# Kernel tuning notes

Measured on AMD Instinct MI355X. Metric: run time of the kernel, lower is better.

Reference implementation:

```python
import jax, jax.numpy as jnp
import numpy as np

NUM_LATENT, NUM_TRASH, DEPTH = 7, 3, 4
N_QUBITS = NUM_LATENT + NUM_TRASH            # 10, embedding/entangler wires
N_WIRES = NUM_LATENT + 2 * NUM_TRASH + 1     # 14, total device wires (wire 0 = MSB, PennyLane convention)
AUX = N_WIRES - 1                            # swap-test ancilla (last wire)
BATCH = 256

_H = (np.array([[1.0, 1.0], [1.0, -1.0]]) / np.sqrt(2.0)).astype(np.complex64)
_CNOT = np.array([[1, 0, 0, 0], [0, 1, 0, 0], [0, 0, 0, 1], [0, 0, 1, 0]], dtype=np.complex64)
_CSWAP = np.eye(8, dtype=np.complex64)
_CSWAP[[5, 6]] = _CSWAP[[6, 5]]              # swap targets iff control=1: |101> <-> |110>


def _rx(theta):
    # RX(theta) = [[cos(t/2), -i sin(t/2)], [-i sin(t/2), cos(t/2)]]; theta [...] -> [..., 2, 2]
    c = jnp.cos(theta / 2).astype(jnp.complex64)
    s = jnp.sin(theta / 2).astype(jnp.complex64) * (-1j)
    return jnp.stack([jnp.stack([c, s], -1), jnp.stack([s, c], -1)], -2)


def _apply_1q(state, gate, wire):
    # state [B, 2^W]; gate [2,2] (shared) or [B,2,2] (per-sample)
    B = state.shape[0]
    a, b = 2 ** wire, 2 ** (N_WIRES - wire - 1)
    s = state.reshape(B, a, 2, b)
    if gate.ndim == 3:
        s = jnp.einsum('bij,bajc->baic', gate, s)
    else:
        s = jnp.einsum('ij,bajc->baic', gate, s)
    return s.reshape(B, -1)


def _apply_kq(state, gate, wires):
    # general k-qubit constant gate on arbitrary (possibly non-adjacent) wires
    B = state.shape[0]
    k = len(wires)
    t = state.reshape((B,) + (2,) * N_WIRES)
    t = jnp.moveaxis(t, [w + 1 for w in wires], range(1, k + 1))
    t = t.reshape(B, 2 ** k, -1)
    t = jnp.einsum('ij,bjc->bic', jnp.asarray(gate), t)
    t = t.reshape((B,) + (2,) * N_WIRES)
    t = jnp.moveaxis(t, range(1, k + 1), [w + 1 for w in wires])
    return t.reshape(B, -1)


def _forward(features, weights):
    B = features.shape[0]
    state = jnp.zeros((B, 2 ** N_WIRES), jnp.complex64).at[:, 0].set(1.0)
    # AngleEmbedding(rotation='X'): per-sample RX(features[:, w]) on wire w
    g_emb = _rx(features)  # [B, n_qubits, 2, 2]
    for w in range(N_QUBITS):
        state = _apply_1q(state, g_emb[:, w], w)
    # BasicEntanglerLayers: per layer, RX(weights[l, w]) on each wire, then ring of CNOTs
    wts = weights.reshape(DEPTH, N_QUBITS)
    for l in range(DEPTH):
        g_l = _rx(wts[l])  # [n_qubits, 2, 2]
        for w in range(N_QUBITS):
            state = _apply_1q(state, g_l[w], w)
        for w in range(N_QUBITS):
            state = _apply_kq(state, _CNOT, [w, (w + 1) % N_QUBITS])
    # Swap test: H(aux); CSWAP(aux, latent+i, latent+trash+i); H(aux)
    state = _apply_1q(state, jnp.asarray(_H), AUX)
    for i in range(NUM_TRASH):
        state = _apply_kq(state, _CSWAP, [AUX, NUM_LATENT + i, NUM_LATENT + NUM_TRASH + i])
    state = _apply_1q(state, jnp.asarray(_H), AUX)
    # probs on aux wire (last wire -> innermost axis); return P(aux=1)
    p = jnp.sum(jnp.abs(state.reshape(B, 2 ** (N_WIRES - 1), 2)) ** 2, axis=1)
    return p[:, 1]


def setup_inputs() -> dict:
    key = jax.random.key(0)
    kf, kw = jax.random.split(key)
    features = jax.random.normal(kf, (BATCH, N_QUBITS), jnp.float32)
    weights = 0.01 * jax.random.uniform(kw, (DEPTH, N_QUBITS), jnp.float32)
    return {"features": features, "weights": weights}


def reference(features, weights):
    return _forward(features, weights)
```

## Files before the change

### kernel.cpp

```cpp
#include <hip/hip_runtime.h>
#include <math.h>


#define NQ     10
#define DEPTHL 4
#define NGATE  (NQ + DEPTHL * NQ)

constexpr int lfwd_step(int i) {
    for (int w = 0; w < NQ; ++w) {
        int cb = (i >> (NQ - 1 - w)) & 1;
        i ^= cb << (NQ - 1 - ((w + 1) % NQ));
    }
    return i;
}
constexpr int linv_step(int i) {
    for (int w = NQ - 1; w >= 0; --w) {
        int cb = (i >> (NQ - 1 - w)) & 1;
        i ^= cb << (NQ - 1 - ((w + 1) % NQ));
    }
    return i;
}

static_assert(lfwd_step(linv_step(0x155)) == 0x155, "linv must invert lfwd");
static_assert(linv_step(lfwd_step(0x2AB)) == 0x2AB, "lfwd must invert linv");

struct MaskTab { int m[NGATE]; int row[3]; };

constexpr MaskTab make_masks() {
    MaskTab M{};
    for (int w = 0; w < NQ; ++w) M.m[w] = 1 << (NQ - 1 - w);
    for (int l = 0; l < DEPTHL; ++l)
        for (int w = 0; w < NQ; ++w) {
            int v = 1 << (NQ - 1 - w);
            for (int k = 0; k < l; ++k) v = linv_step(v);
            M.m[NQ + NQ * l + w] = v;
        }
    for (int p = 0; p < 3; ++p) {
        int r = 0;
        for (int j = 0; j < NQ; ++j) {
            int y = 1 << j;
            for (int k = 0; k < DEPTHL; ++k) y = lfwd_step(y);
            r |= ((y >> p) & 1) << j;
        }
        M.row[p] = r;
    }
    return M;
}

constexpr MaskTab MK = make_masks();

constexpr bool masks_ok() {
    for (int g = 0; g < NGATE; ++g)
        if (MK.m[g] <= 0 || MK.m[g] > 1023) return false;
    return MK.row[0] && MK.row[1] && MK.row[2];
}
static_assert(masks_ok(), "gate masks must be nonzero 10-bit");

__global__ __launch_bounds__(64) void qae_kernel(
    const float* __restrict__ features,
    const float* __restrict__ weights,
    float* __restrict__ out)
{
    const int b    = blockIdx.x;
    const int lane = threadIdx.x;

    float cg = 1.0f, sg = 0.0f;
    if (lane < NGATE) {
        float ang = (lane < NQ) ? features[b * NQ + lane] : weights[lane - NQ];
        float h = 0.5f * ang;
        cg = cosf(h);
        sg = sinf(h);
    }

    float tre[16], tim[16];
#pragma unroll
    for (int r = 0; r < 16; ++r) { tre[r] = 0.0f; tim[r] = 0.0f; }
    if (lane == 0) tre[0] = 1.0f;

#pragma unroll
    for (int g = 0; g < NGATE; ++g) {
        const int v  = MK.m[g];
        const int lm = v >> 4;
        const int rm = v & 15;
        const float c = __shfl(cg, g, 64);
        const float s = __shfl(sg, g, 64);

        float pre[16], pim[16];
        if (lm) {
#pragma unroll
            for (int r = 0; r < 16; ++r) {
                pre[r] = __shfl_xor(tre[r ^ rm], lm, 64);
                pim[r] = __shfl_xor(tim[r ^ rm], lm, 64);
            }
        } else {
#pragma unroll
            for (int r = 0; r < 16; ++r) {
                pre[r] = tre[r ^ rm];
                pim[r] = tim[r ^ rm];
            }
        }
#pragma unroll
        for (int r = 0; r < 16; ++r) {
            tre[r] = fmaf(c, tre[r],  s * pim[r]);
            tim[r] = fmaf(c, tim[r], -s * pre[r]);
        }
    }

    const int pl0 = __popc((MK.row[0] >> 4) & lane) & 1;
    const int pl1 = __popc((MK.row[1] >> 4) & lane) & 1;
    const int pl2 = __popc((MK.row[2] >> 4) & lane) & 1;

    float acc = 0.0f;
#pragma unroll
    for (int r = 0; r < 16; ++r) {
        const int pr0 = __popc(MK.row[0] & 15 & r) & 1;
        const int pr1 = __popc(MK.row[1] & 15 & r) & 1;
        const int pr2 = __popc(MK.row[2] & 15 & r) & 1;
        const int bad = (pl0 ^ pr0) | (pl1 ^ pr1) | (pl2 ^ pr2);
        if (!bad) acc += tre[r] * tre[r] + tim[r] * tim[r];
    }

#pragma unroll
    for (int off = 32; off; off >>= 1)
        acc += __shfl_xor(acc, off, 64);

    if (lane == 0) out[b] = 0.5f * (1.0f - acc);
}

extern "C" void kernel_launch(void* const* d_in, const int* in_sizes, int n_in,
                              void* d_out, int out_size, void* d_ws, size_t ws_size,
                              hipStream_t stream) {
    const float* features = (const float*)d_in[0];
    const float* weights  = (const float*)d_in[1];
    float*       out      = (float*)d_out;

    int B = in_sizes[0] / NQ;
    qae_kernel<<<B, 64, 0, stream>>>(features, weights, out);
}
```

Measured before the change: 64.67 us.

## Replace sequential gate simulation with closed-form phase computation in Fourier basis

Instead of applying fifty RX gates one after another with cross-lane shuffles, the kernel computes each basis amplitude's phase directly as a signed sum of the rotation angles, using parity masks, followed by one sincos per amplitude. It then folds the three measurement parity rows with a few xor-shuffle butterfly additions before summing the squared magnitudes with a normalization factor. This removes about fifty rounds of 32 shuffles plus FMAs, at the cost of per-lane popcount/sign arithmetic and 16 sincos calls. It depends on the Fourier-domain identity holding exactly, and any numerical drift in the phase sums could affect accuracy.

```diff
diff --git a/kernel.cpp b/kernel.cpp
--- a/kernel.cpp
+++ b/kernel.cpp
@@ -4,7 +4,7 @@
 
 #define NQ     10
 #define DEPTHL 4
-#define NGATE  (NQ + DEPTHL * NQ)
+#define NSLOT  (NQ + DEPTHL * NQ)
 
 constexpr int lfwd_step(int i) {
     for (int w = 0; w < NQ; ++w) {
@@ -20,11 +20,10 @@
     }
     return i;
 }
-
 static_assert(lfwd_step(linv_step(0x155)) == 0x155, "linv must invert lfwd");
 static_assert(linv_step(lfwd_step(0x2AB)) == 0x2AB, "lfwd must invert linv");
 
-struct MaskTab { int m[NGATE]; int row[3]; };
+struct MaskTab { int m[NSLOT]; int row[3]; };
 
 constexpr MaskTab make_masks() {
     MaskTab M{};
@@ -46,15 +45,20 @@
     }
     return M;
 }
-
 constexpr MaskTab MK = make_masks();
 
 constexpr bool masks_ok() {
-    for (int g = 0; g < NGATE; ++g)
+    for (int g = 0; g < NSLOT; ++g)
         if (MK.m[g] <= 0 || MK.m[g] > 1023) return false;
     return MK.row[0] && MK.row[1] && MK.row[2];
 }
 static_assert(masks_ok(), "gate masks must be nonzero 10-bit");
+
+constexpr bool rows_indep() {
+    int a = MK.row[0], b = MK.row[1], c = MK.row[2];
+    return a && b && c && (a ^ b) && (a ^ c) && (b ^ c) && (a ^ b ^ c);
+}
+static_assert(rows_indep(), "measurement rows must be linearly independent");
 
 __global__ __launch_bounds__(64) void qae_kernel(
     const float* __restrict__ features,
@@ -64,67 +68,66 @@
     const int b    = blockIdx.x;
     const int lane = threadIdx.x;
 
-    float cg = 1.0f, sg = 0.0f;
-    if (lane < NGATE) {
-        float ang = (lane < NQ) ? features[b * NQ + lane] : weights[lane - NQ];
-        float h = 0.5f * ang;
-        cg = cosf(h);
-        sg = sinf(h);
+    float phi[16];
+#pragma unroll
+    for (int r = 0; r < 16; ++r) phi[r] = 0.0f;
+
+#pragma unroll
+    for (int t = 0; t < NSLOT; ++t) {
+        const int v = MK.m[t];
+        const float th = (t < NQ) ? features[b * NQ + t] : weights[t - NQ];
+        const int par = __popc((v >> 4) & lane) & 1;
+        const float tv = par ? -th : th;
+#pragma unroll
+        for (int r = 0; r < 16; ++r) {
+            if (__popc(v & 15 & r) & 1) phi[r] -= tv;
+            else                        phi[r] += tv;
+        }
     }
 
-    float tre[16], tim[16];
+    float zr[16], zi[16];
 #pragma unroll
-    for (int r = 0; r < 16; ++r) { tre[r] = 0.0f; tim[r] = 0.0f; }
-    if (lane == 0) tre[0] = 1.0f;
+    for (int r = 0; r < 16; ++r) {
+        float sv, cv;
+        sincosf(0.5f * phi[r], &sv, &cv);
+        zr[r] = cv;
+        zi[r] = sv;
+    }
 
 #pragma unroll
-    for (int g = 0; g < NGATE; ++g) {
-        const int v  = MK.m[g];
-        const int lm = v >> 4;
-        const int rm = v & 15;
-        const float c = __shfl(cg, g, 64);
-        const float s = __shfl(sg, g, 64);
-
-        float pre[16], pim[16];
-        if (lm) {
+    for (int p = 0; p < 3; ++p) {
+        const int w  = MK.row[p];
+        const int wl = w >> 4;
+        const int wr = w & 15;
+        float tr[16], ti[16];
+        if (wl) {
 #pragma unroll
             for (int r = 0; r < 16; ++r) {
-                pre[r] = __shfl_xor(tre[r ^ rm], lm, 64);
-                pim[r] = __shfl_xor(tim[r ^ rm], lm, 64);
+                tr[r] = __shfl_xor(zr[r ^ wr], wl, 64);
+                ti[r] = __shfl_xor(zi[r ^ wr], wl, 64);
             }
         } else {
 #pragma unroll
             for (int r = 0; r < 16; ++r) {
-                pre[r] = tre[r ^ rm];
-                pim[r] = tim[r ^ rm];
+                tr[r] = zr[r ^ wr];
+                ti[r] = zi[r ^ wr];
             }
         }
 #pragma unroll
-        for (int r = 0; r < 16; ++r) {
-            tre[r] = fmaf(c, tre[r],  s * pim[r]);
-            tim[r] = fmaf(c, tim[r], -s * pre[r]);
-        }
+        for (int r = 0; r < 16; ++r) { zr[r] += tr[r]; zi[r] += ti[r]; }
     }
-
-    const int pl0 = __popc((MK.row[0] >> 4) & lane) & 1;
-    const int pl1 = __popc((MK.row[1] >> 4) & lane) & 1;
-    const int pl2 = __popc((MK.row[2] >> 4) & lane) & 1;
 
     float acc = 0.0f;
 #pragma unroll
-    for (int r = 0; r < 16; ++r) {
-        const int pr0 = __popc(MK.row[0] & 15 & r) & 1;
-        const int pr1 = __popc(MK.row[1] & 15 & r) & 1;
-        const int pr2 = __popc(MK.row[2] & 15 & r) & 1;
-        const int bad = (pl0 ^ pr0) | (pl1 ^ pr1) | (pl2 ^ pr2);
-        if (!bad) acc += tre[r] * tre[r] + tim[r] * tim[r];
-    }
+    for (int r = 0; r < 16; ++r)
+        acc = fmaf(zr[r], zr[r], fmaf(zi[r], zi[r], acc));
 
 #pragma unroll
     for (int off = 32; off; off >>= 1)
         acc += __shfl_xor(acc, off, 64);
 
-    if (lane == 0) out[b] = 0.5f * (1.0f - acc);
+    if (lane == 0)
+        out[b] = 0.5f * (1.0f - acc * (1.0f / 65536.0f));
 }
 
 extern "C" void kernel_launch(void* const* d_in, const int* in_sizes, int n_in,
```

Result: faster. 58.36 us (-9.8%).
